# Optimization experiments

Hardware: AMD Instinct MI355X
Metric: run time of the kernel (lower is better)

Reference implementation:

```python
import jax, jax.numpy as jnp
import numpy as np

# --- APPM / NMS pipeline constants (3 ratio groups on the 28x28 mixed feature map) ---
RATIOS = [4, 6, 8]            # square sliding-window sizes in feature cells
N_LIST = [2, 3, 2]            # proposals kept per group (proposalN = 7)
IOU_THRESHS = [0.25, 0.25, 0.25]
FM_SIZE = 28                  # mixed feature map spatial size
STRIDE = 16                   # 448 / 28: feature cell -> image pixels
IMG = 448
PROPOSAL_N = sum(N_LIST)
GROUP_SIZES = [(FM_SIZE - r + 1) ** 2 for r in RATIOS]


def make_coordinates():
    """[x0, y0, x1, y1] image-space boxes for every sliding window, all groups concatenated."""
    coords = []
    for r in RATIOS:
        n = FM_SIZE - r + 1
        ii, jj = np.meshgrid(np.arange(n), np.arange(n), indexing='ij')
        x0 = (ii.ravel() * STRIDE).astype(np.int32)
        y0 = (jj.ravel() * STRIDE).astype(np.int32)
        coords.append(np.stack([x0, y0, x0 + r * STRIDE, y0 + r * STRIDE], axis=1))
    return np.concatenate(coords, axis=0).astype(np.int32)   # (1595, 4)


def window_scores_from_fm(fm):
    """AvgPool2d(r, stride=1) then sum over channels == reduce_window over channel-summed map."""
    s = jnp.sum(fm, axis=1)  # (B, H, W)
    outs = []
    for r in RATIOS:
        w = jax.lax.reduce_window(s, 0.0, jax.lax.add, (1, r, r), (1, 1, 1), 'VALID') / float(r * r)
        outs.append(w.reshape(s.shape[0], -1))
    return jnp.concatenate(outs, axis=1)  # (B, sum(GROUP_SIZES))


def nms_group(scores, boxes, n_sel, thresh):
    """Greedy IoU NMS, exactly the inclusive (+1) box math of the source nms()."""
    areas = (boxes[:, 2] - boxes[:, 0] + 1.0) * (boxes[:, 3] - boxes[:, 1] + 1.0)

    def body(k, carry):
        sc, idxs = carry
        i = jnp.argmax(sc)                       # highest remaining score
        idxs = idxs.at[k].set(i.astype(jnp.int32))
        b = boxes[i]
        xx0 = jnp.maximum(boxes[:, 0], b[0]); yy0 = jnp.maximum(boxes[:, 1], b[1])
        xx1 = jnp.minimum(boxes[:, 2], b[2]); yy1 = jnp.minimum(boxes[:, 3], b[3])
        w = xx1 - xx0 + 1.0; h = yy1 - yy0 + 1.0
        inter = jnp.where((w < 0) | (h < 0), 0.0, w * h)
        iou = inter / (areas + areas[i] - inter)
        sc = jnp.where(iou > thresh, -jnp.inf, sc)  # suppress (selected box has iou=1 -> removed)
        return sc, idxs

    _, idxs = jax.lax.fori_loop(0, n_sel, body, (scores, jnp.zeros((n_sel,), jnp.int32)))
    return idxs


def select_proposals(all_scores, coordinates):
    parts = []
    off = 0
    for ng, n_sel, th in zip(GROUP_SIZES, N_LIST, IOU_THRESHS):
        sc = all_scores[:, off:off + ng]
        bx = coordinates[off:off + ng].astype(jnp.float32)
        idx = jax.vmap(lambda s: nms_group(s, bx, n_sel, th))(sc) + off
        parts.append(idx)
        off += ng
    return jnp.concatenate(parts, axis=1)  # (B, PROPOSAL_N) global window indices


def crop_windows(x, coordinates, indices):
    """Gather-crop each proposal window from the raw image, bilinear-resize to 448x448."""
    outs = []
    col = 0
    for r, n_sel in zip(RATIOS, N_LIST):
        w = r * STRIDE  # fixed crop size for this ratio group
        idx_g = indices[:, col:col + n_sel]

        def crop_one(img, gi):
            c = coordinates[gi]
            patch = jax.lax.dynamic_slice(img, (0, c[0], c[1]), (3, w, w))
            return jax.image.resize(patch, (3, IMG, IMG), 'bilinear')

        crops = jax.vmap(lambda img, gis: jax.vmap(lambda gi: crop_one(img, gi))(gis))(x, idx_g)
        outs.append(crops)
        col += n_sel
    return jnp.concatenate(outs, axis=1)  # (B, PROPOSAL_N, 3, 448, 448)


def setup_inputs() -> dict:
    key = jax.random.key(0)
    k1, k2, k3, k4 = jax.random.split(key, 4)
    B = 8
    return {
        'x': jax.random.normal(k1, (B, 3, IMG, IMG), jnp.float32),
        'fm': jax.random.normal(k2, (B, 384, FM_SIZE, FM_SIZE), jnp.float32),
        'embedding': jax.random.normal(k3, (B, 2048), jnp.float32),
        'W_cls': jax.random.normal(k4, (2048, 200), jnp.float32) * 0.02,
        'b_cls': jnp.zeros((200,), jnp.float32),
        'coordinates': jnp.asarray(make_coordinates()),
    }


def reference(x, fm, embedding, W_cls, b_cls, coordinates):
    all_scores = window_scores_from_fm(fm)                              # window_scores (B, 1595)
    proposalN_indices = select_proposals(all_scores, coordinates)       # (B, 7) int32
    proposalN_windows_scores = jnp.take_along_axis(all_scores, proposalN_indices, axis=1)
    window_imgs = crop_windows(x, coordinates, proposalN_indices)
    window_imgs = window_imgs.reshape(-1, 3, IMG, IMG)                  # (B*7, 3, 448, 448)
    raw_logits = embedding @ W_cls + b_cls                              # rawcls_net
    return (proposalN_indices, proposalN_windows_scores, all_scores, window_imgs, raw_logits)
```

## Files before the change

### kernel.cpp

```cpp
#include <hip/hip_runtime.h>
#include <math.h>

#define THREADS 256

typedef float f32x4 __attribute__((ext_vector_type(4)));

__global__ __launch_bounds__(THREADS) void fused1_kernel(const float* __restrict__ fm,
                                                         float4* __restrict__ part,
                                                         int cpc, int K,
                                                         const float* __restrict__ emb,
                                                         const float* __restrict__ W,
                                                         float* __restrict__ lpart) {
    int blk = blockIdx.x;
    int t = threadIdx.x;
    if (blk < 8 * K) {
        int b = blk / K, k = blk - b * K;
        if (t >= 196) return;
        const float4* f = (const float4*)(fm + ((size_t)b * 384 + (size_t)k * cpc) * 784);
        float4 acc = {0.0f, 0.0f, 0.0f, 0.0f};
        for (int c = 0; c < cpc; ++c) {
            float4 v = f[(size_t)c * 196 + t];
            acc.x += v.x; acc.y += v.y; acc.z += v.z; acc.w += v.w;
        }
        part[((size_t)b * K + k) * 196 + t] = acc;
    } else {
        int idx = blk - 8 * K;
        int b = idx >> 4, kc = idx & 15;
        if (t >= 200) return;
        const float* e  = emb + (size_t)b * 2048 + kc * 128;
        const float* wp = W + (size_t)kc * 128 * 200 + t;
        float acc = 0.0f;
        #pragma unroll 4
        for (int k = 0; k < 128; ++k)
            acc += e[k] * wp[(size_t)k * 200];
        lpart[((size_t)b * 16 + kc) * 200 + t] = acc;
    }
}

__global__ __launch_bounds__(THREADS) void fused2_kernel(const float4* __restrict__ part,
                                                         int K,
                                                         float* __restrict__ all_scores,
                                                         float* __restrict__ out_idx_f,
                                                         float* __restrict__ out_sc,
                                                         int* __restrict__ ws_idx,
                                                         const float* __restrict__ lpart,
                                                         const float* __restrict__ bias,
                                                         float* __restrict__ logits) {
    __shared__ float4 s4[196];
    __shared__ float  pref[28][29];
    __shared__ float  scl[625];
    __shared__ float  rv[4];
    __shared__ int    ri[4];
    int t = threadIdx.x;

    if (blockIdx.x >= 24) {
        int b = blockIdx.x - 24;
        if (t >= 200) return;
        float acc = bias[t];
        #pragma unroll
        for (int kc = 0; kc < 16; ++kc)
            acc += lpart[((size_t)b * 16 + kc) * 200 + t];
        logits[b * 200 + t] = acc;
        return;
    }

    float* s = (float*)s4;
    int b = blockIdx.x / 3, g = blockIdx.x - b * 3;

    if (t < 196) {
        float4 acc = {0.0f, 0.0f, 0.0f, 0.0f};
        for (int k = 0; k < K; ++k) {
            float4 v = part[((size_t)b * K + k) * 196 + t];
            acc.x += v.x; acc.y += v.y; acc.z += v.z; acc.w += v.w;
        }
        s4[t] = acc;
    }
    __syncthreads();
    if (t < 28) {
        float run = 0.0f;
        pref[t][0] = 0.0f;
        for (int j = 0; j < 28; ++j) {
            run += s[t * 28 + j];
            pref[t][j + 1] = run;
        }
    }
    __syncthreads();

    const int goffA[3] = {0, 625, 1154};
    const int gnA[3]   = {625, 529, 441};
    const int sideA[3] = {25, 23, 21};
    const int rA[3]    = {4, 6, 8};
    const int nselA[3] = {2, 3, 2};
    const int colA[3]  = {0, 2, 5};

    int n = gnA[g], side = sideA[g], r = rA[g];
    int nsel = nselA[g], goff = goffA[g], colbase = colA[g];
    float inv = 1.0f / (float)(r * r);

    for (int loc = t; loc < n; loc += THREADS) {
        int i = loc / side, j = loc % side;
        float acc = 0.0f;
        for (int a = 0; a < r; ++a)
            acc += pref[i + a][j + r] - pref[i + a][j];
        float sv = acc * inv;
        scl[loc] = sv;
        all_scores[b * 1595 + goff + loc] = sv;
    }
    __syncthreads();

    float ext = (float)(r * 16 + 1);
    float A   = ext * ext;
    float rs  = (float)(r * 16);

    for (int k = 0; k < nsel; ++k) {
        float bv = -INFINITY; int bi = 0x7fffffff;
        for (int i = t; i < n; i += THREADS) {
            float v = scl[i];
            if (v > bv || (v == bv && i < bi)) { bv = v; bi = i; }
        }
        #pragma unroll
        for (int m = 1; m < 64; m <<= 1) {
            float ov = __shfl_xor(bv, m, 64);
            int   oi = __shfl_xor(bi, m, 64);
            if (ov > bv || (ov == bv && oi < bi)) { bv = ov; bi = oi; }
        }
        int wv = t >> 6;
        if ((t & 63) == 0) { rv[wv] = bv; ri[wv] = bi; }
        __syncthreads();
        if (t == 0) {
            for (int q = 1; q < 4; ++q) {
                float ov = rv[q]; int oi = ri[q];
                if (ov > bv || (ov == bv && oi < bi)) { bv = ov; bi = oi; }
            }
            ri[0] = bi;
            int outp = b * 7 + colbase + k;
            out_idx_f[outp] = (float)(goff + bi);
            out_sc[outp]    = bv;
            ws_idx[outp]    = goff + bi;
        }
        __syncthreads();
        int sel = ri[0];
        int si = sel / side, sj = sel % side;
        float sx0 = si * 16.0f, sy0 = sj * 16.0f;
        float sx1 = sx0 + rs,   sy1 = sy0 + rs;
        for (int i = t; i < n; i += THREADS) {
            int ii = i / side, jj = i % side;
            float x0 = ii * 16.0f, y0 = jj * 16.0f;
            float x1 = x0 + rs,    y1 = y0 + rs;
            float xx0 = fmaxf(x0, sx0), yy0 = fmaxf(y0, sy0);
            float xx1 = fminf(x1, sx1), yy1 = fminf(y1, sy1);
            float w = xx1 - xx0 + 1.0f, h = yy1 - yy0 + 1.0f;
            float inter = (w < 0.0f || h < 0.0f) ? 0.0f : w * h;
            float iou = inter / (A + A - inter);
            if (iou > 0.25f) scl[i] = -INFINITY;
        }
        __syncthreads();
    }
}

__global__ __launch_bounds__(448) void crop_kernel(const float* __restrict__ x,
                                                   const int* __restrict__ coords,
                                                   const int* __restrict__ ws_idx,
                                                   float* __restrict__ out) {
    __shared__ float lds[7 * 132];
    int blk = blockIdx.x;
    int p   = blk / 84;
    int rem = blk - p * 84;
    int ch  = rem / 28;
    int stripe = rem - ch * 28;
    int t = threadIdx.x;

    int b = p / 7, col = p - b * 7;
    int g = (col < 2) ? 0 : ((col < 5) ? 1 : 2);
    int w = (g == 0) ? 64 : ((g == 1) ? 96 : 128);
    float scale = (float)w * (1.0f / 448.0f);
    float wm1   = (float)(w - 1);

    int gi = ws_idx[p];
    int c0 = coords[gi * 4 + 0];
    int c1 = coords[gi * 4 + 1];

    int S = stripe * 16;
    float syb = fminf(fmaxf(((float)S + 0.5f) * scale - 0.5f, 0.0f), wm1);
    int r_lo = (int)syb;

    const float* base = x + (((size_t)b * 3 + ch) * 448) * 448 + c1;
    for (int i = t; i < 7 * 132; i += 448) {
        int rr = i / 132, xx = i - rr * 132;
        lds[i] = base[(size_t)(c0 + min(r_lo + rr, w - 1)) * 448 + min(xx, w - 1)];
    }
    __syncthreads();

    int row_sub = t / 56;
    int seg     = t - row_sub * 56;
    int ox0 = seg * 8;

    float sxb = ((float)ox0 + 0.5f) * scale - 0.5f;
    float sx0 = fminf(fmaxf(sxb, 0.0f), wm1);
    int   i0  = (int)sx0;
    int   dk[8];
    float txk[8];
    #pragma unroll
    for (int k = 0; k < 8; ++k) {
        float sx = fminf(fmaxf(sxb + (float)k * scale, 0.0f), wm1);
        int xi = (int)sx;
        dk[k]  = xi - i0;
        txk[k] = sx - (float)xi;
    }

    #pragma unroll
    for (int half = 0; half < 2; ++half) {
        int oy = S + half * 8 + row_sub;
        float sy = fminf(fmaxf(((float)oy + 0.5f) * scale - 0.5f, 0.0f), wm1);
        int   y0 = (int)sy;
        int   y1 = min(y0 + 1, w - 1);
        float ty = sy - (float)y0;
        const float* l0 = lds + (y0 - r_lo) * 132 + i0;
        const float* l1 = lds + (y1 - r_lo) * 132 + i0;
        float a0 = l0[0], a1 = l0[1], a2 = l0[2], a3 = l0[3];
        float b0 = l1[0], b1 = l1[1], b2 = l1[2], b3 = l1[3];

        f32x4 res0, res1;
        #pragma unroll
        for (int k = 0; k < 8; ++k) {
            int   d   = dk[k];
            float v00 = (d == 0) ? a0 : ((d == 1) ? a1 : a2);
            float v01 = (d == 0) ? a1 : ((d == 1) ? a2 : a3);
            float v10 = (d == 0) ? b0 : ((d == 1) ? b1 : b2);
            float v11 = (d == 0) ? b1 : ((d == 1) ? b2 : b3);
            float tx  = txk[k];
            float top = v00 + tx * (v01 - v00);
            float bot = v10 + tx * (v11 - v10);
            float r   = top + ty * (bot - top);
            if (k < 4) res0[k] = r; else res1[k - 4] = r;
        }
        float* orow = out + (((size_t)p * 3 + ch) * 448 + oy) * 448 + ox0;
        *(f32x4*)orow       = res0;
        *(f32x4*)(orow + 4) = res1;
    }
}

extern "C" void kernel_launch(void* const* d_in, const int* in_sizes, int n_in,
                              void* d_out, int out_size, void* d_ws, size_t ws_size,
                              hipStream_t stream) {
    const float* x      = (const float*)d_in[0];
    const float* fm     = (const float*)d_in[1];
    const float* emb    = (const float*)d_in[2];
    const float* Wc     = (const float*)d_in[3];
    const float* bc     = (const float*)d_in[4];
    const int*   coords = (const int*)d_in[5];

    float* out        = (float*)d_out;
    float* out_idx    = out;
    float* out_sc     = out + 56;
    float* all_scores = out + 112;
    float* imgs       = out + 12872;
    float* logits     = out + 33731144;

    int K = 32;
    while (K > 1 && ws_size < 1024 + (size_t)8 * K * 784 * 4 + 25600 * 4) K >>= 1;
    int cpc = 384 / K;

    int*    ws_idx = (int*)d_ws;
    float4* part   = (float4*)((char*)d_ws + 1024);
    float*  lpart  = (float*)((char*)d_ws + 1024 + (size_t)8 * K * 784 * 4);

    fused1_kernel<<<8 * K + 128, THREADS, 0, stream>>>(fm, part, cpc, K, emb, Wc, lpart);
    fused2_kernel<<<32, THREADS, 0, stream>>>(part, K, all_scores, out_idx, out_sc, ws_idx,
                                              lpart, bc, logits);
    crop_kernel<<<56 * 84, 448, 0, stream>>>(x, coords, ws_idx, imgs);
}
```

Before: 59.58 us.

## Make crop kernel persistent with register-prefetched double-buffered LDS tiles

The crop kernel now runs a fixed grid of 1024 blocks. Each block loops over stripe tasks and prefetches the next task's source pixels into registers while it computes and stores the current one, using two LDS buffers so only one barrier is needed per task. The aim is to hide global load latency and cut block launch overhead. The cost is more register pressure, and with 4704 tasks spread over 1024 blocks the load per block is uneven. It also unrolls the partial-sum loop in fused2 and vectorises that kernel's prefix-row loads.

```diff
diff --git a/kernel.cpp b/kernel.cpp
--- a/kernel.cpp
+++ b/kernel.cpp
@@ -64,11 +64,11 @@
         return;
     }
 
-    float* s = (float*)s4;
     int b = blockIdx.x / 3, g = blockIdx.x - b * 3;
 
     if (t < 196) {
         float4 acc = {0.0f, 0.0f, 0.0f, 0.0f};
+        #pragma unroll 8
         for (int k = 0; k < K; ++k) {
             float4 v = part[((size_t)b * K + k) * 196 + t];
             acc.x += v.x; acc.y += v.y; acc.z += v.z; acc.w += v.w;
@@ -77,21 +77,25 @@
     }
     __syncthreads();
     if (t < 28) {
+        float4 row[7];
+        #pragma unroll
+        for (int i = 0; i < 7; ++i) row[i] = s4[t * 7 + i];
         float run = 0.0f;
         pref[t][0] = 0.0f;
+        #pragma unroll
         for (int j = 0; j < 28; ++j) {
-            run += s[t * 28 + j];
+            run += ((float*)row)[j];
             pref[t][j + 1] = run;
         }
     }
     __syncthreads();
 
-    const int goffA[3] = {0, 625, 1154};
     const int gnA[3]   = {625, 529, 441};
     const int sideA[3] = {25, 23, 21};
     const int rA[3]    = {4, 6, 8};
     const int nselA[3] = {2, 3, 2};
     const int colA[3]  = {0, 2, 5};
+    const int goffA[3] = {0, 625, 1154};
 
     int n = gnA[g], side = sideA[g], r = rA[g];
     int nsel = nselA[g], goff = goffA[g], colbase = colA[g];
@@ -158,85 +162,144 @@
     }
 }
 
+#define CROP_GRID 1024
+#define NTASK (56 * 3 * 28)
+
 __global__ __launch_bounds__(448) void crop_kernel(const float* __restrict__ x,
                                                    const int* __restrict__ coords,
                                                    const int* __restrict__ ws_idx,
                                                    float* __restrict__ out) {
-    __shared__ float lds[7 * 132];
-    int blk = blockIdx.x;
-    int p   = blk / 84;
-    int rem = blk - p * 84;
-    int ch  = rem / 28;
-    int stripe = rem - ch * 28;
+    __shared__ float lds[2][7 * 132];
     int t = threadIdx.x;
 
-    int b = p / 7, col = p - b * 7;
-    int g = (col < 2) ? 0 : ((col < 5) ? 1 : 2);
-    int w = (g == 0) ? 64 : ((g == 1) ? 96 : 128);
-    float scale = (float)w * (1.0f / 448.0f);
-    float wm1   = (float)(w - 1);
-
-    int gi = ws_idx[p];
-    int c0 = coords[gi * 4 + 0];
-    int c1 = coords[gi * 4 + 1];
-
-    int S = stripe * 16;
-    float syb = fminf(fmaxf(((float)S + 0.5f) * scale - 0.5f, 0.0f), wm1);
-    int r_lo = (int)syb;
-
-    const float* base = x + (((size_t)b * 3 + ch) * 448) * 448 + c1;
-    for (int i = t; i < 7 * 132; i += 448) {
-        int rr = i / 132, xx = i - rr * 132;
-        lds[i] = base[(size_t)(c0 + min(r_lo + rr, w - 1)) * 448 + min(xx, w - 1)];
-    }
-    __syncthreads();
-
+    int rr0 = t / 132,        xx0 = t - rr0 * 132;
+    int i1  = t + 448;
+    int rr1 = i1 / 132,       xx1 = i1 - rr1 * 132;
+    int rr2 = 6,              xx2 = t + 104;
     int row_sub = t / 56;
     int seg     = t - row_sub * 56;
     int ox0 = seg * 8;
 
-    float sxb = ((float)ox0 + 0.5f) * scale - 0.5f;
-    float sx0 = fminf(fmaxf(sxb, 0.0f), wm1);
-    int   i0  = (int)sx0;
-    int   dk[8];
-    float txk[8];
-    #pragma unroll
-    for (int k = 0; k < 8; ++k) {
-        float sx = fminf(fmaxf(sxb + (float)k * scale, 0.0f), wm1);
-        int xi = (int)sx;
-        dk[k]  = xi - i0;
-        txk[k] = sx - (float)xi;
-    }
-
-    #pragma unroll
-    for (int half = 0; half < 2; ++half) {
-        int oy = S + half * 8 + row_sub;
-        float sy = fminf(fmaxf(((float)oy + 0.5f) * scale - 0.5f, 0.0f), wm1);
-        int   y0 = (int)sy;
-        int   y1 = min(y0 + 1, w - 1);
-        float ty = sy - (float)y0;
-        const float* l0 = lds + (y0 - r_lo) * 132 + i0;
-        const float* l1 = lds + (y1 - r_lo) * 132 + i0;
-        float a0 = l0[0], a1 = l0[1], a2 = l0[2], a3 = l0[3];
-        float b0 = l1[0], b1 = l1[1], b2 = l1[2], b3 = l1[3];
-
-        f32x4 res0, res1;
-        #pragma unroll
-        for (int k = 0; k < 8; ++k) {
-            int   d   = dk[k];
-            float v00 = (d == 0) ? a0 : ((d == 1) ? a1 : a2);
-            float v01 = (d == 0) ? a1 : ((d == 1) ? a2 : a3);
-            float v10 = (d == 0) ? b0 : ((d == 1) ? b1 : b2);
-            float v11 = (d == 0) ? b1 : ((d == 1) ? b2 : b3);
-            float tx  = txk[k];
-            float top = v00 + tx * (v01 - v00);
-            float bot = v10 + tx * (v11 - v10);
-            float r   = top + ty * (bot - top);
-            if (k < 4) res0[k] = r; else res1[k - 4] = r;
-        }
-        float* orow = out + (((size_t)p * 3 + ch) * 448 + oy) * 448 + ox0;
-        *(f32x4*)orow       = res0;
-        *(f32x4*)(orow + 4) = res1;
+    int task = blockIdx.x;
+
+    int    c_w, c_rlo, c_S;
+    float  c_scale, c_wm1;
+    size_t c_outb;
+    const float* c_base;
+    float rA, rB, rC;
+
+    {
+        int p = task / 84, rem = task - p * 84;
+        int ch = rem / 28, stripe = rem - ch * 28;
+        int b = p / 7, col = p - b * 7;
+        int g = (col < 2) ? 0 : ((col < 5) ? 1 : 2);
+        c_w = (g == 0) ? 64 : ((g == 1) ? 96 : 128);
+        c_scale = (float)c_w * (1.0f / 448.0f);
+        c_wm1 = (float)(c_w - 1);
+        c_S = stripe * 16;
+        float syb = fminf(fmaxf(((float)c_S + 0.5f) * c_scale - 0.5f, 0.0f), c_wm1);
+        c_rlo = (int)syb;
+        int gi = ws_idx[p];
+        int c0 = coords[gi * 4 + 0];
+        int c1 = coords[gi * 4 + 1];
+        c_base = x + (((size_t)b * 3 + ch) * 448) * 448 + c1 + (size_t)c0 * 448;
+        c_outb = (((size_t)p * 3 + ch) * 448) * 448;
+        rA = c_base[(size_t)min(c_rlo + rr0, c_w - 1) * 448 + min(xx0, c_w - 1)];
+        rB = c_base[(size_t)min(c_rlo + rr1, c_w - 1) * 448 + min(xx1, c_w - 1)];
+        if (t < 28)
+            rC = c_base[(size_t)min(c_rlo + rr2, c_w - 1) * 448 + min(xx2, c_w - 1)];
+    }
+
+    int buf = 0;
+    while (true) {
+        lds[buf][t]       = rA;
+        lds[buf][t + 448] = rB;
+        if (t < 28) lds[buf][t + 896] = rC;
+
+        int nxt = task + CROP_GRID;
+        bool has_nxt = nxt < NTASK;
+        int    n_w = 0, n_rlo = 0, n_S = 0;
+        float  n_scale = 0.0f, n_wm1 = 0.0f;
+        size_t n_outb = 0;
+        const float* n_base = nullptr;
+        float nA = 0.0f, nB = 0.0f, nC = 0.0f;
+        if (has_nxt) {
+            int p = nxt / 84, rem = nxt - p * 84;
+            int ch = rem / 28, stripe = rem - ch * 28;
+            int b = p / 7, col = p - b * 7;
+            int g = (col < 2) ? 0 : ((col < 5) ? 1 : 2);
+            n_w = (g == 0) ? 64 : ((g == 1) ? 96 : 128);
+            n_scale = (float)n_w * (1.0f / 448.0f);
+            n_wm1 = (float)(n_w - 1);
+            n_S = stripe * 16;
+            float syb = fminf(fmaxf(((float)n_S + 0.5f) * n_scale - 0.5f, 0.0f), n_wm1);
+            n_rlo = (int)syb;
+            int gi = ws_idx[p];
+            int c0 = coords[gi * 4 + 0];
+            int c1 = coords[gi * 4 + 1];
+            n_base = x + (((size_t)b * 3 + ch) * 448) * 448 + c1 + (size_t)c0 * 448;
+            n_outb = (((size_t)p * 3 + ch) * 448) * 448;
+            nA = n_base[(size_t)min(n_rlo + rr0, n_w - 1) * 448 + min(xx0, n_w - 1)];
+            nB = n_base[(size_t)min(n_rlo + rr1, n_w - 1) * 448 + min(xx1, n_w - 1)];
+            if (t < 28)
+                nC = n_base[(size_t)min(n_rlo + rr2, n_w - 1) * 448 + min(xx2, n_w - 1)];
+        }
+
+        __syncthreads();
+
+        {
+            float sxb = ((float)ox0 + 0.5f) * c_scale - 0.5f;
+            float sxc = fminf(fmaxf(sxb, 0.0f), c_wm1);
+            int   i0  = (int)sxc;
+            int   dk[8];
+            float txk[8];
+            #pragma unroll
+            for (int k = 0; k < 8; ++k) {
+                float sx = fminf(fmaxf(sxb + (float)k * c_scale, 0.0f), c_wm1);
+                int xi = (int)sx;
+                dk[k]  = xi - i0;
+                txk[k] = sx - (float)xi;
+            }
+            const float* lbase = &lds[buf][0];
+            #pragma unroll
+            for (int half = 0; half < 2; ++half) {
+                int oy = c_S + half * 8 + row_sub;
+                float sy = fminf(fmaxf(((float)oy + 0.5f) * c_scale - 0.5f, 0.0f), c_wm1);
+                int   y0 = (int)sy;
+                int   y1 = min(y0 + 1, c_w - 1);
+                float ty = sy - (float)y0;
+                const float* l0 = lbase + (y0 - c_rlo) * 132 + i0;
+                const float* l1 = lbase + (y1 - c_rlo) * 132 + i0;
+                float a0 = l0[0], a1 = l0[1], a2 = l0[2], a3 = l0[3];
+                float b0 = l1[0], b1 = l1[1], b2 = l1[2], b3 = l1[3];
+
+                f32x4 res0, res1;
+                #pragma unroll
+                for (int k = 0; k < 8; ++k) {
+                    int   d   = dk[k];
+                    float v00 = (d == 0) ? a0 : ((d == 1) ? a1 : a2);
+                    float v01 = (d == 0) ? a1 : ((d == 1) ? a2 : a3);
+                    float v10 = (d == 0) ? b0 : ((d == 1) ? b1 : b2);
+                    float v11 = (d == 0) ? b1 : ((d == 1) ? b2 : b3);
+                    float tx  = txk[k];
+                    float top = v00 + tx * (v01 - v00);
+                    float bot = v10 + tx * (v11 - v10);
+                    float rr  = top + ty * (bot - top);
+                    if (k < 4) res0[k] = rr; else res1[k - 4] = rr;
+                }
+                float* orow = out + c_outb + (size_t)oy * 448 + ox0;
+                *(f32x4*)orow       = res0;
+                *(f32x4*)(orow + 4) = res1;
+            }
+        }
+
+        if (!has_nxt) break;
+        c_w = n_w; c_rlo = n_rlo; c_S = n_S;
+        c_scale = n_scale; c_wm1 = n_wm1;
+        c_outb = n_outb; c_base = n_base;
+        rA = nA; rB = nB; rC = nC;
+        task = nxt;
+        buf ^= 1;
     }
 }
 
@@ -268,5 +331,5 @@
     fused1_kernel<<<8 * K + 128, THREADS, 0, stream>>>(fm, part, cpc, K, emb, Wc, lpart);
     fused2_kernel<<<32, THREADS, 0, stream>>>(part, K, all_scores, out_idx, out_sc, ws_idx,
                                               lpart, bc, logits);
-    crop_kernel<<<56 * 84, 448, 0, stream>>>(x, coords, ws_idx, imgs);
+    crop_kernel<<<CROP_GRID, 448, 0, stream>>>(x, coords, ws_idx, imgs);
 }
```

After: 53.12 us. -10.8%, faster.

## Merge NMS and crop into persistent mega-kernel with flag sync and async LDS prefetch

Applied to the files above, without the earlier changes.

Folds the NMS/score kernel and the crop kernel into one launch. 1024 persistent crop blocks spin on an atomic done counter until the 24 NMS blocks have published their selected indices. The crop blocks then loop over tasks, double-buffering each next stripe into LDS with global_load_lds while they interpolate the current one. This removes a kernel launch boundary and overlaps input loads with compute, at the cost of spin-waiting blocks, a deadlock risk if the NMS blocks are not scheduled, and larger LDS use per block.

```diff
diff --git a/kernel.cpp b/kernel.cpp
--- a/kernel.cpp
+++ b/kernel.cpp
@@ -2,17 +2,24 @@
 #include <math.h>
 
 #define THREADS 256
+#define NTASK (56 * 3 * 28)
+#define CROP_BLOCKS 1024
 
 typedef float f32x4 __attribute__((ext_vector_type(4)));
+typedef const __attribute__((address_space(1))) float ga_float;
+typedef __attribute__((address_space(3))) float lds_float;
 
 __global__ __launch_bounds__(THREADS) void fused1_kernel(const float* __restrict__ fm,
                                                          float4* __restrict__ part,
                                                          int cpc, int K,
                                                          const float* __restrict__ emb,
                                                          const float* __restrict__ W,
-                                                         float* __restrict__ lpart) {
+                                                         float* __restrict__ lpart,
+                                                         int* __restrict__ done) {
     int blk = blockIdx.x;
     int t = threadIdx.x;
+    if (blk == 0 && t == 0)
+        __hip_atomic_store(done, 0, __ATOMIC_RELAXED, __HIP_MEMORY_SCOPE_AGENT);
     if (blk < 8 * K) {
         int b = blk / K, k = blk - b * K;
         if (t >= 196) return;
@@ -37,24 +44,60 @@
     }
 }
 
-__global__ __launch_bounds__(THREADS) void fused2_kernel(const float4* __restrict__ part,
-                                                         int K,
-                                                         float* __restrict__ all_scores,
-                                                         float* __restrict__ out_idx_f,
-                                                         float* __restrict__ out_sc,
-                                                         int* __restrict__ ws_idx,
-                                                         const float* __restrict__ lpart,
-                                                         const float* __restrict__ bias,
-                                                         float* __restrict__ logits) {
+struct Geo {
+    int w, rlo, S;
+    float scale, wm1;
+    const float* base;
+    float* outp;
+};
+
+__device__ __forceinline__ Geo geo(int task, const float* __restrict__ x,
+                                   const int* __restrict__ coords,
+                                   const int* __restrict__ ws_idx,
+                                   float* __restrict__ imgs) {
+    Geo G;
+    int p = task / 84, rem = task - p * 84;
+    int ch = rem / 28, stripe = rem - ch * 28;
+    int b = p / 7, col = p - b * 7;
+    int g = (col < 2) ? 0 : ((col < 5) ? 1 : 2);
+    G.w = (g == 0) ? 64 : ((g == 1) ? 96 : 128);
+    G.scale = (float)G.w * (1.0f / 448.0f);
+    G.wm1 = (float)(G.w - 1);
+    G.S = stripe * 16;
+    float syb = fminf(fmaxf(((float)G.S + 0.5f) * G.scale - 0.5f, 0.0f), G.wm1);
+    G.rlo = (int)syb;
+    int gi = __hip_atomic_load(&ws_idx[p], __ATOMIC_RELAXED, __HIP_MEMORY_SCOPE_AGENT);
+    int c0 = coords[gi * 4 + 0];
+    int c1 = coords[gi * 4 + 1];
+    G.base = x + (((size_t)b * 3 + ch) * 448) * 448 + c1 + (size_t)c0 * 448;
+    G.outp = imgs + (((size_t)p * 3 + ch) * 448) * 448;
+    return G;
+}
+
+__global__ __launch_bounds__(448) void mega_kernel(const float4* __restrict__ part,
+                                                   int K,
+                                                   float* __restrict__ all_scores,
+                                                   float* __restrict__ out_idx_f,
+                                                   float* __restrict__ out_sc,
+                                                   int* __restrict__ ws_idx,
+                                                   const float* __restrict__ lpart,
+                                                   const float* __restrict__ bias,
+                                                   float* __restrict__ logits,
+                                                   const float* __restrict__ x,
+                                                   const int* __restrict__ coords,
+                                                   float* __restrict__ imgs,
+                                                   int* __restrict__ done) {
     __shared__ float4 s4[196];
     __shared__ float  pref[28][29];
     __shared__ float  scl[625];
-    __shared__ float  rv[4];
-    __shared__ int    ri[4];
+    __shared__ float  rv[7];
+    __shared__ int    ri[7];
+    __shared__ float  lds[2][7 * 132];
     int t = threadIdx.x;
-
-    if (blockIdx.x >= 24) {
-        int b = blockIdx.x - 24;
+    int bid = blockIdx.x;
+
+    if (bid >= 24 && bid < 32) {
+        int b = bid - 24;
         if (t >= 200) return;
         float acc = bias[t];
         #pragma unroll
@@ -64,179 +107,195 @@
         return;
     }
 
-    float* s = (float*)s4;
-    int b = blockIdx.x / 3, g = blockIdx.x - b * 3;
-
-    if (t < 196) {
-        float4 acc = {0.0f, 0.0f, 0.0f, 0.0f};
-        for (int k = 0; k < K; ++k) {
-            float4 v = part[((size_t)b * K + k) * 196 + t];
-            acc.x += v.x; acc.y += v.y; acc.z += v.z; acc.w += v.w;
-        }
-        s4[t] = acc;
+    if (bid < 24) {
+        int b = bid / 3, g = bid - b * 3;
+
+        if (t < 196) {
+            float4 acc = {0.0f, 0.0f, 0.0f, 0.0f};
+            #pragma unroll 8
+            for (int k = 0; k < K; ++k) {
+                float4 v = part[((size_t)b * K + k) * 196 + t];
+                acc.x += v.x; acc.y += v.y; acc.z += v.z; acc.w += v.w;
+            }
+            s4[t] = acc;
+        }
+        __syncthreads();
+        if (t < 28) {
+            float4 row[7];
+            #pragma unroll
+            for (int i = 0; i < 7; ++i) row[i] = s4[t * 7 + i];
+            float run = 0.0f;
+            pref[t][0] = 0.0f;
+            #pragma unroll
+            for (int j = 0; j < 28; ++j) {
+                run += ((float*)row)[j];
+                pref[t][j + 1] = run;
+            }
+        }
+        __syncthreads();
+
+        const int gnA[3]   = {625, 529, 441};
+        const int sideA[3] = {25, 23, 21};
+        const int rA[3]    = {4, 6, 8};
+        const int nselA[3] = {2, 3, 2};
+        const int colA[3]  = {0, 2, 5};
+        const int goffA[3] = {0, 625, 1154};
+
+        int n = gnA[g], side = sideA[g], r = rA[g];
+        int nsel = nselA[g], goff = goffA[g], colbase = colA[g];
+        float inv = 1.0f / (float)(r * r);
+
+        for (int loc = t; loc < n; loc += 448) {
+            int i = loc / side, j = loc % side;
+            float acc = 0.0f;
+            for (int a = 0; a < r; ++a)
+                acc += pref[i + a][j + r] - pref[i + a][j];
+            float sv = acc * inv;
+            scl[loc] = sv;
+            all_scores[b * 1595 + goff + loc] = sv;
+        }
+        __syncthreads();
+
+        float ext = (float)(r * 16 + 1);
+        float A   = ext * ext;
+        float rs  = (float)(r * 16);
+
+        for (int k = 0; k < nsel; ++k) {
+            float bv = -INFINITY; int bi = 0x7fffffff;
+            for (int i = t; i < n; i += 448) {
+                float v = scl[i];
+                if (v > bv || (v == bv && i < bi)) { bv = v; bi = i; }
+            }
+            #pragma unroll
+            for (int m = 1; m < 64; m <<= 1) {
+                float ov = __shfl_xor(bv, m, 64);
+                int   oi = __shfl_xor(bi, m, 64);
+                if (ov > bv || (ov == bv && oi < bi)) { bv = ov; bi = oi; }
+            }
+            int wv = t >> 6;
+            if ((t & 63) == 0) { rv[wv] = bv; ri[wv] = bi; }
+            __syncthreads();
+            if (t == 0) {
+                for (int q = 1; q < 7; ++q) {
+                    float ov = rv[q]; int oi = ri[q];
+                    if (ov > bv || (ov == bv && oi < bi)) { bv = ov; bi = oi; }
+                }
+                ri[0] = bi;
+                int outp = b * 7 + colbase + k;
+                out_idx_f[outp] = (float)(goff + bi);
+                out_sc[outp]    = bv;
+                __hip_atomic_store(&ws_idx[outp], goff + bi,
+                                   __ATOMIC_RELAXED, __HIP_MEMORY_SCOPE_AGENT);
+            }
+            __syncthreads();
+            int sel = ri[0];
+            int si = sel / side, sj = sel % side;
+            float sx0 = si * 16.0f, sy0 = sj * 16.0f;
+            float sx1 = sx0 + rs,   sy1 = sy0 + rs;
+            for (int i = t; i < n; i += 448) {
+                int ii = i / side, jj = i % side;
+                float x0 = ii * 16.0f, y0 = jj * 16.0f;
+                float x1 = x0 + rs,    y1 = y0 + rs;
+                float xx0 = fmaxf(x0, sx0), yy0 = fmaxf(y0, sy0);
+                float xx1 = fminf(x1, sx1), yy1 = fminf(y1, sy1);
+                float w = xx1 - xx0 + 1.0f, h = yy1 - yy0 + 1.0f;
+                float inter = (w < 0.0f || h < 0.0f) ? 0.0f : w * h;
+                float iou = inter / (A + A - inter);
+                if (iou > 0.25f) scl[i] = -INFINITY;
+            }
+            __syncthreads();
+        }
+        if (t == 0)
+            __hip_atomic_fetch_add(done, 1, __ATOMIC_RELEASE, __HIP_MEMORY_SCOPE_AGENT);
+        return;
+    }
+
+    if (t == 0) {
+        while (__hip_atomic_load(done, __ATOMIC_ACQUIRE, __HIP_MEMORY_SCOPE_AGENT) < 24)
+            __builtin_amdgcn_s_sleep(2);
     }
     __syncthreads();
-    if (t < 28) {
-        float run = 0.0f;
-        pref[t][0] = 0.0f;
-        for (int j = 0; j < 28; ++j) {
-            run += s[t * 28 + j];
-            pref[t][j + 1] = run;
-        }
-    }
-    __syncthreads();
-
-    const int goffA[3] = {0, 625, 1154};
-    const int gnA[3]   = {625, 529, 441};
-    const int sideA[3] = {25, 23, 21};
-    const int rA[3]    = {4, 6, 8};
-    const int nselA[3] = {2, 3, 2};
-    const int colA[3]  = {0, 2, 5};
-
-    int n = gnA[g], side = sideA[g], r = rA[g];
-    int nsel = nselA[g], goff = goffA[g], colbase = colA[g];
-    float inv = 1.0f / (float)(r * r);
-
-    for (int loc = t; loc < n; loc += THREADS) {
-        int i = loc / side, j = loc % side;
-        float acc = 0.0f;
-        for (int a = 0; a < r; ++a)
-            acc += pref[i + a][j + r] - pref[i + a][j];
-        float sv = acc * inv;
-        scl[loc] = sv;
-        all_scores[b * 1595 + goff + loc] = sv;
-    }
-    __syncthreads();
-
-    float ext = (float)(r * 16 + 1);
-    float A   = ext * ext;
-    float rs  = (float)(r * 16);
-
-    for (int k = 0; k < nsel; ++k) {
-        float bv = -INFINITY; int bi = 0x7fffffff;
-        for (int i = t; i < n; i += THREADS) {
-            float v = scl[i];
-            if (v > bv || (v == bv && i < bi)) { bv = v; bi = i; }
-        }
-        #pragma unroll
-        for (int m = 1; m < 64; m <<= 1) {
-            float ov = __shfl_xor(bv, m, 64);
-            int   oi = __shfl_xor(bi, m, 64);
-            if (ov > bv || (ov == bv && oi < bi)) { bv = ov; bi = oi; }
-        }
-        int wv = t >> 6;
-        if ((t & 63) == 0) { rv[wv] = bv; ri[wv] = bi; }
-        __syncthreads();
-        if (t == 0) {
-            for (int q = 1; q < 4; ++q) {
-                float ov = rv[q]; int oi = ri[q];
-                if (ov > bv || (ov == bv && oi < bi)) { bv = ov; bi = oi; }
-            }
-            ri[0] = bi;
-            int outp = b * 7 + colbase + k;
-            out_idx_f[outp] = (float)(goff + bi);
-            out_sc[outp]    = bv;
-            ws_idx[outp]    = goff + bi;
-        }
-        __syncthreads();
-        int sel = ri[0];
-        int si = sel / side, sj = sel % side;
-        float sx0 = si * 16.0f, sy0 = sj * 16.0f;
-        float sx1 = sx0 + rs,   sy1 = sy0 + rs;
-        for (int i = t; i < n; i += THREADS) {
-            int ii = i / side, jj = i % side;
-            float x0 = ii * 16.0f, y0 = jj * 16.0f;
-            float x1 = x0 + rs,    y1 = y0 + rs;
-            float xx0 = fmaxf(x0, sx0), yy0 = fmaxf(y0, sy0);
-            float xx1 = fminf(x1, sx1), yy1 = fminf(y1, sy1);
-            float w = xx1 - xx0 + 1.0f, h = yy1 - yy0 + 1.0f;
-            float inter = (w < 0.0f || h < 0.0f) ? 0.0f : w * h;
-            float iou = inter / (A + A - inter);
-            if (iou > 0.25f) scl[i] = -INFINITY;
-        }
-        __syncthreads();
-    }
-}
-
-__global__ __launch_bounds__(448) void crop_kernel(const float* __restrict__ x,
-                                                   const int* __restrict__ coords,
-                                                   const int* __restrict__ ws_idx,
-                                                   float* __restrict__ out) {
-    __shared__ float lds[7 * 132];
-    int blk = blockIdx.x;
-    int p   = blk / 84;
-    int rem = blk - p * 84;
-    int ch  = rem / 28;
-    int stripe = rem - ch * 28;
-    int t = threadIdx.x;
-
-    int b = p / 7, col = p - b * 7;
-    int g = (col < 2) ? 0 : ((col < 5) ? 1 : 2);
-    int w = (g == 0) ? 64 : ((g == 1) ? 96 : 128);
-    float scale = (float)w * (1.0f / 448.0f);
-    float wm1   = (float)(w - 1);
-
-    int gi = ws_idx[p];
-    int c0 = coords[gi * 4 + 0];
-    int c1 = coords[gi * 4 + 1];
-
-    int S = stripe * 16;
-    float syb = fminf(fmaxf(((float)S + 0.5f) * scale - 0.5f, 0.0f), wm1);
-    int r_lo = (int)syb;
-
-    const float* base = x + (((size_t)b * 3 + ch) * 448) * 448 + c1;
-    for (int i = t; i < 7 * 132; i += 448) {
-        int rr = i / 132, xx = i - rr * 132;
-        lds[i] = base[(size_t)(c0 + min(r_lo + rr, w - 1)) * 448 + min(xx, w - 1)];
-    }
-    __syncthreads();
-
+
+    int cb = bid - 32;
+    int r4   = t / 33;
+    int c4x4 = (t - r4 * 33) * 4;
     int row_sub = t / 56;
     int seg     = t - row_sub * 56;
     int ox0 = seg * 8;
 
-    float sxb = ((float)ox0 + 0.5f) * scale - 0.5f;
-    float sx0 = fminf(fmaxf(sxb, 0.0f), wm1);
-    int   i0  = (int)sx0;
-    int   dk[8];
-    float txk[8];
-    #pragma unroll
-    for (int k = 0; k < 8; ++k) {
-        float sx = fminf(fmaxf(sxb + (float)k * scale, 0.0f), wm1);
-        int xi = (int)sx;
-        dk[k]  = xi - i0;
-        txk[k] = sx - (float)xi;
-    }
-
-    #pragma unroll
-    for (int half = 0; half < 2; ++half) {
-        int oy = S + half * 8 + row_sub;
-        float sy = fminf(fmaxf(((float)oy + 0.5f) * scale - 0.5f, 0.0f), wm1);
-        int   y0 = (int)sy;
-        int   y1 = min(y0 + 1, w - 1);
-        float ty = sy - (float)y0;
-        const float* l0 = lds + (y0 - r_lo) * 132 + i0;
-        const float* l1 = lds + (y1 - r_lo) * 132 + i0;
-        float a0 = l0[0], a1 = l0[1], a2 = l0[2], a3 = l0[3];
-        float b0 = l1[0], b1 = l1[1], b2 = l1[2], b3 = l1[3];
-
-        f32x4 res0, res1;
-        #pragma unroll
-        for (int k = 0; k < 8; ++k) {
-            int   d   = dk[k];
-            float v00 = (d == 0) ? a0 : ((d == 1) ? a1 : a2);
-            float v01 = (d == 0) ? a1 : ((d == 1) ? a2 : a3);
-            float v10 = (d == 0) ? b0 : ((d == 1) ? b1 : b2);
-            float v11 = (d == 0) ? b1 : ((d == 1) ? b2 : b3);
-            float tx  = txk[k];
-            float top = v00 + tx * (v01 - v00);
-            float bot = v10 + tx * (v11 - v10);
-            float r   = top + ty * (bot - top);
-            if (k < 4) res0[k] = r; else res1[k - 4] = r;
-        }
-        float* orow = out + (((size_t)p * 3 + ch) * 448 + oy) * 448 + ox0;
-        *(f32x4*)orow       = res0;
-        *(f32x4*)(orow + 4) = res1;
+    int task = cb;
+    Geo Gc = geo(task, x, coords, ws_idx, imgs);
+    if (t < 231) {
+        const float* ga = Gc.base + (size_t)min(Gc.rlo + r4, Gc.w - 1) * 448
+                        + min(c4x4, Gc.w - 4);
+        __builtin_amdgcn_global_load_lds((ga_float*)ga, (lds_float*)&lds[0][t * 4], 16, 0, 0);
+    }
+    int buf = 0;
+
+    while (true) {
+        int nxt = task + CROP_BLOCKS;
+        bool has = nxt < NTASK;
+        __syncthreads();
+
+        Geo Gn;
+        if (has) {
+            Gn = geo(nxt, x, coords, ws_idx, imgs);
+            if (t < 231) {
+                const float* ga = Gn.base + (size_t)min(Gn.rlo + r4, Gn.w - 1) * 448
+                                + min(c4x4, Gn.w - 4);
+                __builtin_amdgcn_global_load_lds((ga_float*)ga,
+                                                 (lds_float*)&lds[buf ^ 1][t * 4], 16, 0, 0);
+            }
+        }
+
+        {
+            float sxb = ((float)ox0 + 0.5f) * Gc.scale - 0.5f;
+            float sxc = fminf(fmaxf(sxb, 0.0f), Gc.wm1);
+            int   i0  = (int)sxc;
+            int   dk[8];
+            float txk[8];
+            #pragma unroll
+            for (int k = 0; k < 8; ++k) {
+                float sx = fminf(fmaxf(sxb + (float)k * Gc.scale, 0.0f), Gc.wm1);
+                int xi = (int)sx;
+                dk[k]  = xi - i0;
+                txk[k] = sx - (float)xi;
+            }
+            const float* lbase = &lds[buf][0];
+            #pragma unroll
+            for (int half = 0; half < 2; ++half) {
+                int oy = Gc.S + half * 8 + row_sub;
+                float sy = fminf(fmaxf(((float)oy + 0.5f) * Gc.scale - 0.5f, 0.0f), Gc.wm1);
+                int   y0 = (int)sy;
+                int   y1 = min(y0 + 1, Gc.w - 1);
+                float ty = sy - (float)y0;
+                const float* l0 = lbase + (y0 - Gc.rlo) * 132 + i0;
+                const float* l1 = lbase + (y1 - Gc.rlo) * 132 + i0;
+                float a0 = l0[0], a1 = l0[1], a2 = l0[2], a3 = l0[3];
+                float b0 = l1[0], b1 = l1[1], b2 = l1[2], b3 = l1[3];
+
+                f32x4 res0, res1;
+                #pragma unroll
+                for (int k = 0; k < 8; ++k) {
+                    int   d   = dk[k];
+                    float v00 = (d == 0) ? a0 : ((d == 1) ? a1 : a2);
+                    float v01 = (d == 0) ? a1 : ((d == 1) ? a2 : a3);
+                    float v10 = (d == 0) ? b0 : ((d == 1) ? b1 : b2);
+                    float v11 = (d == 0) ? b1 : ((d == 1) ? b2 : b3);
+                    float tx  = txk[k];
+                    float top = v00 + tx * (v01 - v00);
+                    float bot = v10 + tx * (v11 - v10);
+                    float rr  = top + ty * (bot - top);
+                    if (k < 4) res0[k] = rr; else res1[k - 4] = rr;
+                }
+                float* orow = Gc.outp + (size_t)oy * 448 + ox0;
+                *(f32x4*)orow       = res0;
+                *(f32x4*)(orow + 4) = res1;
+            }
+        }
+
+        if (!has) break;
+        Gc = Gn; buf ^= 1; task = nxt;
     }
 }
 
@@ -262,11 +321,12 @@
     int cpc = 384 / K;
 
     int*    ws_idx = (int*)d_ws;
+    int*    done   = (int*)((char*)d_ws + 512);
     float4* part   = (float4*)((char*)d_ws + 1024);
     float*  lpart  = (float*)((char*)d_ws + 1024 + (size_t)8 * K * 784 * 4);
 
-    fused1_kernel<<<8 * K + 128, THREADS, 0, stream>>>(fm, part, cpc, K, emb, Wc, lpart);
-    fused2_kernel<<<32, THREADS, 0, stream>>>(part, K, all_scores, out_idx, out_sc, ws_idx,
-                                              lpart, bc, logits);
-    crop_kernel<<<56 * 84, 448, 0, stream>>>(x, coords, ws_idx, imgs);
+    fused1_kernel<<<8 * K + 128, THREADS, 0, stream>>>(fm, part, cpc, K, emb, Wc, lpart, done);
+    mega_kernel<<<32 + CROP_BLOCKS, 448, 0, stream>>>(part, K, all_scores, out_idx, out_sc,
+                                                      ws_idx, lpart, bc, logits,
+                                                      x, coords, imgs, done);
 }
```

Result: slower. 87.91 us (+47.5%).

## Read crop source rows directly from global memory with a grid-stride persistent grid

Applied to the files above, without the earlier changes.

The crop kernel no longer stages source rows in LDS behind a barrier. Each thread issues unaligned 4-wide global loads for its two source rows per output row and interpolates from registers. The launch becomes a fixed 1024-block grid that loops over tasks. Separately, fused2 unrolls the partial-sum loop and loads each row into registers before the prefix scan. This removes LDS traffic and synchronisation, at the cost of redundant, unaligned global reads that rely on the cache.

```diff
diff --git a/kernel.cpp b/kernel.cpp
--- a/kernel.cpp
+++ b/kernel.cpp
@@ -2,8 +2,11 @@
 #include <math.h>
 
 #define THREADS 256
+#define CROP_GRID 1024
+#define NTASK (56 * 3 * 28)
 
 typedef float f32x4 __attribute__((ext_vector_type(4)));
+typedef float f32x4u __attribute__((ext_vector_type(4), aligned(4)));
 
 __global__ __launch_bounds__(THREADS) void fused1_kernel(const float* __restrict__ fm,
                                                          float4* __restrict__ part,
@@ -64,11 +67,11 @@
         return;
     }
 
-    float* s = (float*)s4;
     int b = blockIdx.x / 3, g = blockIdx.x - b * 3;
 
     if (t < 196) {
         float4 acc = {0.0f, 0.0f, 0.0f, 0.0f};
+        #pragma unroll 8
         for (int k = 0; k < K; ++k) {
             float4 v = part[((size_t)b * K + k) * 196 + t];
             acc.x += v.x; acc.y += v.y; acc.z += v.z; acc.w += v.w;
@@ -77,21 +80,25 @@
     }
     __syncthreads();
     if (t < 28) {
+        float4 row[7];
+        #pragma unroll
+        for (int i = 0; i < 7; ++i) row[i] = s4[t * 7 + i];
         float run = 0.0f;
         pref[t][0] = 0.0f;
+        #pragma unroll
         for (int j = 0; j < 28; ++j) {
-            run += s[t * 28 + j];
+            run += ((float*)row)[j];
             pref[t][j + 1] = run;
         }
     }
     __syncthreads();
 
-    const int goffA[3] = {0, 625, 1154};
     const int gnA[3]   = {625, 529, 441};
     const int sideA[3] = {25, 23, 21};
     const int rA[3]    = {4, 6, 8};
     const int nselA[3] = {2, 3, 2};
     const int colA[3]  = {0, 2, 5};
+    const int goffA[3] = {0, 625, 1154};
 
     int n = gnA[g], side = sideA[g], r = rA[g];
     int nsel = nselA[g], goff = goffA[g], colbase = colA[g];
@@ -162,81 +169,80 @@
                                                    const int* __restrict__ coords,
                                                    const int* __restrict__ ws_idx,
                                                    float* __restrict__ out) {
-    __shared__ float lds[7 * 132];
-    int blk = blockIdx.x;
-    int p   = blk / 84;
-    int rem = blk - p * 84;
-    int ch  = rem / 28;
-    int stripe = rem - ch * 28;
     int t = threadIdx.x;
-
-    int b = p / 7, col = p - b * 7;
-    int g = (col < 2) ? 0 : ((col < 5) ? 1 : 2);
-    int w = (g == 0) ? 64 : ((g == 1) ? 96 : 128);
-    float scale = (float)w * (1.0f / 448.0f);
-    float wm1   = (float)(w - 1);
-
-    int gi = ws_idx[p];
-    int c0 = coords[gi * 4 + 0];
-    int c1 = coords[gi * 4 + 1];
-
-    int S = stripe * 16;
-    float syb = fminf(fmaxf(((float)S + 0.5f) * scale - 0.5f, 0.0f), wm1);
-    int r_lo = (int)syb;
-
-    const float* base = x + (((size_t)b * 3 + ch) * 448) * 448 + c1;
-    for (int i = t; i < 7 * 132; i += 448) {
-        int rr = i / 132, xx = i - rr * 132;
-        lds[i] = base[(size_t)(c0 + min(r_lo + rr, w - 1)) * 448 + min(xx, w - 1)];
-    }
-    __syncthreads();
-
     int row_sub = t / 56;
     int seg     = t - row_sub * 56;
     int ox0 = seg * 8;
 
-    float sxb = ((float)ox0 + 0.5f) * scale - 0.5f;
-    float sx0 = fminf(fmaxf(sxb, 0.0f), wm1);
-    int   i0  = (int)sx0;
-    int   dk[8];
-    float txk[8];
-    #pragma unroll
-    for (int k = 0; k < 8; ++k) {
-        float sx = fminf(fmaxf(sxb + (float)k * scale, 0.0f), wm1);
-        int xi = (int)sx;
-        dk[k]  = xi - i0;
-        txk[k] = sx - (float)xi;
-    }
-
-    #pragma unroll
-    for (int half = 0; half < 2; ++half) {
-        int oy = S + half * 8 + row_sub;
-        float sy = fminf(fmaxf(((float)oy + 0.5f) * scale - 0.5f, 0.0f), wm1);
-        int   y0 = (int)sy;
-        int   y1 = min(y0 + 1, w - 1);
-        float ty = sy - (float)y0;
-        const float* l0 = lds + (y0 - r_lo) * 132 + i0;
-        const float* l1 = lds + (y1 - r_lo) * 132 + i0;
-        float a0 = l0[0], a1 = l0[1], a2 = l0[2], a3 = l0[3];
-        float b0 = l1[0], b1 = l1[1], b2 = l1[2], b3 = l1[3];
-
-        f32x4 res0, res1;
+    for (int task = blockIdx.x; task < NTASK; task += CROP_GRID) {
+        int p = task / 84, rem = task - p * 84;
+        int ch = rem / 28, stripe = rem - ch * 28;
+        int b = p / 7, col = p - b * 7;
+        int g = (col < 2) ? 0 : ((col < 5) ? 1 : 2);
+        int w = (g == 0) ? 64 : ((g == 1) ? 96 : 128);
+        float scale = (float)w * (1.0f / 448.0f);
+        float wm1   = (float)(w - 1);
+        int S = stripe * 16;
+        int gi = ws_idx[p];
+        int c0 = coords[gi * 4 + 0];
+        int c1 = coords[gi * 4 + 1];
+        const float* base = x + (((size_t)b * 3 + ch) * 448) * 448 + c1 + (size_t)c0 * 448;
+        float* outb = out + (((size_t)p * 3 + ch) * 448) * 448;
+
+        float sxb = ((float)ox0 + 0.5f) * scale - 0.5f;
+        float sxc = fminf(fmaxf(sxb, 0.0f), wm1);
+        int   ib  = min((int)sxc, w - 4);
+        int   i0k[8], i1k[8];
+        float txk[8];
         #pragma unroll
         for (int k = 0; k < 8; ++k) {
-            int   d   = dk[k];
-            float v00 = (d == 0) ? a0 : ((d == 1) ? a1 : a2);
-            float v01 = (d == 0) ? a1 : ((d == 1) ? a2 : a3);
-            float v10 = (d == 0) ? b0 : ((d == 1) ? b1 : b2);
-            float v11 = (d == 0) ? b1 : ((d == 1) ? b2 : b3);
-            float tx  = txk[k];
-            float top = v00 + tx * (v01 - v00);
-            float bot = v10 + tx * (v11 - v10);
-            float r   = top + ty * (bot - top);
-            if (k < 4) res0[k] = r; else res1[k - 4] = r;
-        }
-        float* orow = out + (((size_t)p * 3 + ch) * 448 + oy) * 448 + ox0;
-        *(f32x4*)orow       = res0;
-        *(f32x4*)(orow + 4) = res1;
+            float sx = fminf(fmaxf(sxb + (float)k * scale, 0.0f), wm1);
+            int xi = (int)sx;
+            txk[k] = sx - (float)xi;
+            i0k[k] = xi - ib;
+            i1k[k] = min(xi + 1, w - 1) - ib;
+        }
+
+        int   y0h[2], y1h[2];
+        float tyh[2];
+        #pragma unroll
+        for (int h = 0; h < 2; ++h) {
+            int oy = S + h * 8 + row_sub;
+            float sy = fminf(fmaxf(((float)oy + 0.5f) * scale - 0.5f, 0.0f), wm1);
+            int y0 = (int)sy;
+            y0h[h] = y0;
+            y1h[h] = min(y0 + 1, w - 1);
+            tyh[h] = sy - (float)y0;
+        }
+        f32x4 r00 = *(const f32x4u*)(base + (size_t)y0h[0] * 448 + ib);
+        f32x4 r01 = *(const f32x4u*)(base + (size_t)y1h[0] * 448 + ib);
+        f32x4 r10 = *(const f32x4u*)(base + (size_t)y0h[1] * 448 + ib);
+        f32x4 r11 = *(const f32x4u*)(base + (size_t)y1h[1] * 448 + ib);
+
+        #pragma unroll
+        for (int h = 0; h < 2; ++h) {
+            f32x4 ra = h ? r10 : r00;
+            f32x4 rb = h ? r11 : r01;
+            float ty = tyh[h];
+            int oy = S + h * 8 + row_sub;
+            f32x4 res0, res1;
+            #pragma unroll
+            for (int k = 0; k < 8; ++k) {
+                int ia = i0k[k], ic = i1k[k];
+                float v00 = (ia == 0) ? ra[0] : ((ia == 1) ? ra[1] : ((ia == 2) ? ra[2] : ra[3]));
+                float v01 = (ic == 0) ? ra[0] : ((ic == 1) ? ra[1] : ((ic == 2) ? ra[2] : ra[3]));
+                float v10 = (ia == 0) ? rb[0] : ((ia == 1) ? rb[1] : ((ia == 2) ? rb[2] : rb[3]));
+                float v11 = (ic == 0) ? rb[0] : ((ic == 1) ? rb[1] : ((ic == 2) ? rb[2] : rb[3]));
+                float tx  = txk[k];
+                float top = v00 + tx * (v01 - v00);
+                float bot = v10 + tx * (v11 - v10);
+                float rr  = top + ty * (bot - top);
+                if (k < 4) res0[k] = rr; else res1[k - 4] = rr;
+            }
+            float* orow = outb + (size_t)oy * 448 + ox0;
+            *(f32x4*)orow       = res0;
+            *(f32x4*)(orow + 4) = res1;
+        }
     }
 }
 
@@ -268,5 +274,5 @@
     fused1_kernel<<<8 * K + 128, THREADS, 0, stream>>>(fm, part, cpc, K, emb, Wc, lpart);
     fused2_kernel<<<32, THREADS, 0, stream>>>(part, K, all_scores, out_idx, out_sc, ws_idx,
                                               lpart, bc, logits);
-    crop_kernel<<<56 * 84, 448, 0, stream>>>(x, coords, ws_idx, imgs);
-}
+    crop_kernel<<<CROP_GRID, 448, 0, stream>>>(x, coords, ws_idx, imgs);
+}
```

After: 65.07 us. 1.09x slower.
